# Kernel optimization log

Hardware: AMD Instinct MI355X
Metric: run time of the kernel (lower is better)

The kernel has to match this reference:

```python
import jax, jax.numpy as jnp
import numpy as np


def xenet_batch(x, a, e, sw, sb, aiw, aib, ajw, ajb, nw, nb, ew, eb):
    """Spektral XENetConvBatch: x (B,N,F), a (B,N,N), e (B,N,N,S)."""
    B, N, F = x.shape
    x_i = jnp.broadcast_to(x[:, :, None, :], (B, N, N, F))   # target node i per pair
    x_j = jnp.broadcast_to(x[:, None, :, :], (B, N, N, F))   # source node j per pair
    e_t = jnp.transpose(e, (0, 2, 1, 3))                      # reversed edge features
    stack = jnp.concatenate([x_i, x_j, e, e_t], axis=-1)      # (B,N,N,2F+2S)
    stack = jax.nn.relu(stack @ sw + sb)                      # stack MLP, (B,N,N,32)
    stack = stack * a[..., None]                              # mask/weight by adjacency
    att_i = jax.nn.sigmoid(stack @ aiw + aib)                 # incoming gate
    att_j = jax.nn.sigmoid(stack @ ajw + ajb)                 # outgoing gate
    agg_i = jnp.sum(att_i * stack, axis=2)                    # aggregate over sources j -> (B,N,32)
    agg_j = jnp.sum(att_j * stack, axis=1)                    # aggregate over targets i -> (B,N,32)
    x_out = jnp.concatenate([x, agg_i, agg_j], axis=-1) @ nw + nb  # node model (linear)
    e_out = stack @ ew + eb                                   # edge model (linear)
    return x_out, e_out


def setup_inputs() -> dict:
    key = jax.random.key(0)
    ks = jax.random.split(key, 16)
    B, N, F, S, C, L = 1, 400, 240, 1, 32, 1440
    SIN = 2 * F + 2 * S   # 482
    NIN = F + 2 * C       # 304
    s = 0.05
    inp = {
        "x": jax.random.normal(ks[0], (B, N, F), jnp.float32),
        "a": jax.random.uniform(ks[1], (B, N, N), jnp.float32),
        "e": jax.random.normal(ks[2], (B, N, N, S), jnp.float32),
        "c1_sw": jax.random.normal(ks[3], (SIN, C), jnp.float32) * s,
        "c1_sb": jnp.zeros((C,), jnp.float32),
        "c1_aiw": jax.random.normal(ks[4], (C, 1), jnp.float32) * s,
        "c1_aib": jnp.zeros((1,), jnp.float32),
        "c1_ajw": jax.random.normal(ks[5], (C, 1), jnp.float32) * s,
        "c1_ajb": jnp.zeros((1,), jnp.float32),
        "c1_nw": jax.random.normal(ks[6], (NIN, F), jnp.float32) * s,
        "c1_nb": jnp.zeros((F,), jnp.float32),
        "c1_ew": jax.random.normal(ks[7], (C, S), jnp.float32) * s,
        "c1_eb": jnp.zeros((S,), jnp.float32),
        "c2_sw": jax.random.normal(ks[8], (SIN, C), jnp.float32) * s,
        "c2_sb": jnp.zeros((C,), jnp.float32),
        "c2_aiw": jax.random.normal(ks[9], (C, 1), jnp.float32) * s,
        "c2_aib": jnp.zeros((1,), jnp.float32),
        "c2_ajw": jax.random.normal(ks[10], (C, 1), jnp.float32) * s,
        "c2_ajb": jnp.zeros((1,), jnp.float32),
        "c2_nw": jax.random.normal(ks[11], (NIN, F), jnp.float32) * s,
        "c2_nb": jnp.zeros((F,), jnp.float32),
        "c2_ew": jax.random.normal(ks[12], (C, S), jnp.float32) * s,
        "c2_eb": jnp.zeros((S,), jnp.float32),
        "dw": jax.random.normal(ks[13], (F, L), jnp.float32) * s,
        "db": jnp.zeros((L,), jnp.float32),
    }
    return inp


def reference(x, a, e,
              c1_sw, c1_sb, c1_aiw, c1_aib, c1_ajw, c1_ajb, c1_nw, c1_nb, c1_ew, c1_eb,
              c2_sw, c2_sb, c2_aiw, c2_aib, c2_ajw, c2_ajb, c2_nw, c2_nb, c2_ew, c2_eb,
              dw, db):
    x, e = xenet_batch(x, a, e, c1_sw, c1_sb, c1_aiw, c1_aib, c1_ajw, c1_ajb,
                       c1_nw, c1_nb, c1_ew, c1_eb)
    x, e = xenet_batch(x, a, e, c2_sw, c2_sb, c2_aiw, c2_aib, c2_ajw, c2_ajb,
                       c2_nw, c2_nb, c2_ew, c2_eb)
    return x @ dw + db  # (B, N, n_labels)
```

## Files before the change

### kernel.cpp

```cpp
#include <hip/hip_runtime.h>

#define NN 400
#define FF 240
#define CC 32
#define NIN 304
#define LL 1440

__global__ __launch_bounds__(256) void pq_kernel(
    const float* __restrict__ x, const float* __restrict__ sw,
    const float* __restrict__ sb, float* __restrict__ P, float* __restrict__ Q) {
    const int i   = blockIdx.x;
    const int t   = threadIdx.x;
    const int c   = t & 31;
    const int isQ = (t >> 5) & 1;
    const int g   = t >> 6;
    const float* wb = sw + (isQ ? FF * CC : 0) + c;
    float acc = (!isQ && g == 0) ? sb[c] : 0.0f;
    const float* xr = x + i * FF;
    const int f0 = g * 60;
    #pragma unroll 4
    for (int f = f0; f < f0 + 60; ++f) acc += xr[f] * wb[f * CC];
    __shared__ float red[4][64];
    red[g][t & 63] = acc;
    __syncthreads();
    if (t < 64) {
        const float s = red[0][t] + red[1][t] + red[2][t] + red[3][t];
        if (t >= 32) Q[i * CC + (t & 31)] = s;
        else         P[i * CC + t] = s;
    }
}

template<bool WRITE_E, bool DO_PQ>
__global__ __launch_bounds__(1024) void rcf_node(
    const float* __restrict__ P, const float* __restrict__ Q,
    const float* __restrict__ e, const float* __restrict__ a,
    const float* __restrict__ sw_tail,
    const float* __restrict__ aiw, const float* __restrict__ aib,
    const float* __restrict__ ajw, const float* __restrict__ ajb,
    const float* __restrict__ ew, const float* __restrict__ eb,
    float* __restrict__ e_out,
    const float* __restrict__ xin, const float* __restrict__ nw,
    const float* __restrict__ nb,
    const float* __restrict__ sw2, const float* __restrict__ sb2,
    float* __restrict__ xout, float* __restrict__ Pout, float* __restrict__ Qout) {
    const int bid = blockIdx.x;
    const int b   = (bid & 7) * 50 + (bid >> 3);
    const int t  = threadIdx.x;
    const int pg = t >> 3, l = t & 7, c0 = l * 4;

    __shared__ float smem[10272];
    float* red  = smem;
    float* v    = smem + 9216;
    float* xs   = smem + 9520;
    float* part = smem + 9760;
    float* redn = smem;
    float* red2 = smem;

    if (t < FF) v[t] = xin[b * FF + t];

    float e_f4[4], e_r4[4], a_bk4[4], a_kb4[4];
    int kk[4];
    #pragma unroll
    for (int it = 0; it < 4; ++it) {
        const int off = it * 128 + pg;
        kk[it] = (off < NN) ? off : 0;
        e_f4[it]  = e[b * NN + kk[it]];
        e_r4[it]  = e[kk[it] * NN + b];
        a_bk4[it] = a[b * NN + kk[it]];
        a_kb4[it] = a[kk[it] * NN + b];
    }

    float w1v[4], w2v[4], wiv[4], wjv[4], wev[4], Pb[4], Qb[4];
    *(float4*)w1v = *(const float4*)(sw_tail + c0);
    *(float4*)w2v = *(const float4*)(sw_tail + CC + c0);
    *(float4*)wiv = *(const float4*)(aiw + c0);
    *(float4*)wjv = *(const float4*)(ajw + c0);
    if (WRITE_E) *(float4*)wev = *(const float4*)(ew + c0);
    *(float4*)Pb = *(const float4*)(P + b * CC + c0);
    *(float4*)Qb = *(const float4*)(Q + b * CC + c0);
    const float bi = aib[0], bj = ajb[0];
    const float be = WRITE_E ? eb[0] : 0.0f;

    float acc_i[4] = {0, 0, 0, 0}, acc_j[4] = {0, 0, 0, 0};
    #pragma unroll
    for (int it = 0; it < 4; ++it) {
        const int off = it * 128 + pg;
        const bool valid = off < NN;
        const int k = kk[it];
        float Qk[4], Pk[4];
        *(float4*)Qk = *(const float4*)(Q + k * CC + c0);
        *(float4*)Pk = *(const float4*)(P + k * CC + c0);
        const float e_f = e_f4[it], e_r = e_r4[it];
        const float a_bk = a_bk4[it], a_kb = a_kb4[it];
        float sr[4], sc[4];
        #pragma unroll
        for (int q = 0; q < 4; ++q) {
            sr[q] = fmaxf(Pb[q] + Qk[q] + e_f * w1v[q] + e_r * w2v[q], 0.0f) * a_bk;
            sc[q] = fmaxf(Pk[q] + Qb[q] + e_r * w1v[q] + e_f * w2v[q], 0.0f) * a_kb;
        }
        float d_i = sr[0] * wiv[0] + sr[1] * wiv[1] + sr[2] * wiv[2] + sr[3] * wiv[3];
        float d_j = sc[0] * wjv[0] + sc[1] * wjv[1] + sc[2] * wjv[2] + sc[3] * wjv[3];
        float d_e = WRITE_E ? (sr[0] * wev[0] + sr[1] * wev[1] + sr[2] * wev[2] + sr[3] * wev[3]) : 0.0f;
        #pragma unroll
        for (int m = 1; m < 8; m <<= 1) {
            d_i += __shfl_xor(d_i, m);
            d_j += __shfl_xor(d_j, m);
            if (WRITE_E) d_e += __shfl_xor(d_e, m);
        }
        const float gi = valid ? __fdividef(1.0f, 1.0f + __expf(-(d_i + bi))) : 0.0f;
        const float gj = valid ? __fdividef(1.0f, 1.0f + __expf(-(d_j + bj))) : 0.0f;
        #pragma unroll
        for (int q = 0; q < 4; ++q) {
            acc_i[q] += gi * sr[q];
            acc_j[q] += gj * sc[q];
        }
        if (WRITE_E && l == 0 && valid) e_out[b * NN + k] = d_e + be;
    }
    #pragma unroll
    for (int q = 0; q < 4; ++q) {
        red[pg * 36 + c0 + q]          = acc_i[q];
        red[(128 + pg) * 36 + c0 + q]  = acc_j[q];
    }
    __syncthreads();
    if (t < 512) {
        const int c = t & 31, sg = (t >> 5) & 7, which = t >> 8;
        float s = 0.0f;
        #pragma unroll
        for (int g2 = sg * 16; g2 < sg * 16 + 16; ++g2)
            s += red[(which * 128 + g2) * 36 + c];
        part[t] = s;
    }
    __syncthreads();
    if (t < 64) {
        const int which = t >> 5, c = t & 31;
        float s = 0.0f;
        #pragma unroll
        for (int sg = 0; sg < 8; ++sg) s += part[which * 256 + sg * 32 + c];
        v[FF + t] = s;
    }
    __syncthreads();

    {
        const int fg = t % 60, h = t / 60;
        if (t < 960) {
            const int f0 = fg * 4;
            float4 acc = make_float4(0.f, 0.f, 0.f, 0.f);
            const int k0 = h * 19;
            #pragma unroll
            for (int k = k0; k < k0 + 19; ++k) {
                const float vk = v[k];
                const float4 w = *(const float4*)(nw + k * FF + f0);
                acc.x += vk * w.x; acc.y += vk * w.y;
                acc.z += vk * w.z; acc.w += vk * w.w;
            }
            *(float4*)(redn + h * 240 + f0) = acc;
        }
    }
    __syncthreads();
    if (t < FF) {
        float r = nb[t];
        #pragma unroll
        for (int h = 0; h < 16; ++h) r += redn[h * 240 + t];
        xout[b * FF + t] = r;
        xs[t] = r;
    }
    if (DO_PQ) {
        __syncthreads();
        const int c = t & 31, isQ = (t >> 5) & 1, g = t >> 6;
        const float* wb = sw2 + (isQ ? FF * CC : 0) + c;
        float acc = (!isQ && g == 0) ? sb2[c] : 0.0f;
        const int f0 = g * 15;
        #pragma unroll
        for (int f = f0; f < f0 + 15; ++f) acc += xs[f] * wb[f * CC];
        red2[g * 64 + (t & 63)] = acc;
        __syncthreads();
        if (t < 64) {
            float s = 0.0f;
            #pragma unroll
            for (int g2 = 0; g2 < 16; ++g2) s += red2[g2 * 64 + t];
            if (t >= 32) Qout[b * CC + (t & 31)] = s;
            else         Pout[b * CC + t] = s;
        }
    }
}

__global__ __launch_bounds__(256) void dense_kernel(
    const float* __restrict__ x, const float* __restrict__ dw,
    const float* __restrict__ db, float* __restrict__ out) {
    const int i0 = blockIdx.x * 8;
    const int l  = blockIdx.y * 256 + threadIdx.x;
    __shared__ float xs[8][FF];
    for (int idx = threadIdx.x; idx < 8 * FF; idx += 256) {
        const int r = idx / FF, f = idx - r * FF;
        xs[r][f] = x[(i0 + r) * FF + f];
    }
    __syncthreads();
    if (l < LL) {
        float a0 = db[l], a1 = a0, a2 = a0, a3 = a0;
        float a4 = a0, a5 = a0, a6 = a0, a7 = a0;
        #pragma unroll 4
        for (int f = 0; f < FF; ++f) {
            const float w = dw[f * LL + l];
            a0 += xs[0][f] * w;
            a1 += xs[1][f] * w;
            a2 += xs[2][f] * w;
            a3 += xs[3][f] * w;
            a4 += xs[4][f] * w;
            a5 += xs[5][f] * w;
            a6 += xs[6][f] * w;
            a7 += xs[7][f] * w;
        }
        out[(i0 + 0) * LL + l] = a0;
        out[(i0 + 1) * LL + l] = a1;
        out[(i0 + 2) * LL + l] = a2;
        out[(i0 + 3) * LL + l] = a3;
        out[(i0 + 4) * LL + l] = a4;
        out[(i0 + 5) * LL + l] = a5;
        out[(i0 + 6) * LL + l] = a6;
        out[(i0 + 7) * LL + l] = a7;
    }
}

extern "C" void kernel_launch(void* const* d_in, const int* in_sizes, int n_in,
                              void* d_out, int out_size, void* d_ws, size_t ws_size,
                              hipStream_t stream) {
    const float* x  = (const float*)d_in[0];
    const float* a  = (const float*)d_in[1];
    const float* e0 = (const float*)d_in[2];

    const float* c1_sw  = (const float*)d_in[3];
    const float* c1_sb  = (const float*)d_in[4];
    const float* c1_aiw = (const float*)d_in[5];
    const float* c1_aib = (const float*)d_in[6];
    const float* c1_ajw = (const float*)d_in[7];
    const float* c1_ajb = (const float*)d_in[8];
    const float* c1_nw  = (const float*)d_in[9];
    const float* c1_nb  = (const float*)d_in[10];
    const float* c1_ew  = (const float*)d_in[11];
    const float* c1_eb  = (const float*)d_in[12];

    const float* c2_sw  = (const float*)d_in[13];
    const float* c2_sb  = (const float*)d_in[14];
    const float* c2_aiw = (const float*)d_in[15];
    const float* c2_aib = (const float*)d_in[16];
    const float* c2_ajw = (const float*)d_in[17];
    const float* c2_ajb = (const float*)d_in[18];
    const float* c2_nw  = (const float*)d_in[19];
    const float* c2_nb  = (const float*)d_in[20];
    const float* dw = (const float*)d_in[23];
    const float* db = (const float*)d_in[24];

    float* ws = (float*)d_ws;
    float* P1 = ws;
    float* Q1 = ws + 12800;
    float* P2 = ws + 25600;
    float* Q2 = ws + 38400;
    float* x1 = ws + 51200;
    float* x2 = ws + 147200;
    float* e1 = ws + 243200;

    float* out = (float*)d_out;

    pq_kernel<<<NN, 256, 0, stream>>>(x, c1_sw, c1_sb, P1, Q1);

    rcf_node<true, true><<<NN, 1024, 0, stream>>>(
        P1, Q1, e0, a, c1_sw + 480 * CC,
        c1_aiw, c1_aib, c1_ajw, c1_ajb, c1_ew, c1_eb, e1,
        x, c1_nw, c1_nb, c2_sw, c2_sb, x1, P2, Q2);

    rcf_node<false, false><<<NN, 1024, 0, stream>>>(
        P2, Q2, e1, a, c2_sw + 480 * CC,
        c2_aiw, c2_aib, c2_ajw, c2_ajb, nullptr, nullptr, nullptr,
        x1, c2_nw, c2_nb, nullptr, nullptr, x2, nullptr, nullptr);

    dense_kernel<<<dim3(NN / 8, 6), 256, 0, stream>>>(x2, dw, db, out);
}
```

Measured before the change: 62.42 us.

## Process two nodes per block to share weight reads in node kernels

Each block of the PQ and fused edge/node kernels now handles two target nodes instead of one, halving grid size. The node-model and next-layer PQ weight loads are shared across both nodes, cutting global/L2 weight traffic per node. The edge aggregation phase runs sequentially for the two nodes with extra barriers, and fewer blocks may leave compute units idle.

```diff
diff --git a/kernel.cpp b/kernel.cpp
--- a/kernel.cpp
+++ b/kernel.cpp
@@ -9,24 +9,34 @@
 __global__ __launch_bounds__(256) void pq_kernel(
     const float* __restrict__ x, const float* __restrict__ sw,
     const float* __restrict__ sb, float* __restrict__ P, float* __restrict__ Q) {
-    const int i   = blockIdx.x;
+    const int i0  = blockIdx.x * 2;
     const int t   = threadIdx.x;
     const int c   = t & 31;
     const int isQ = (t >> 5) & 1;
     const int g   = t >> 6;
     const float* wb = sw + (isQ ? FF * CC : 0) + c;
-    float acc = (!isQ && g == 0) ? sb[c] : 0.0f;
-    const float* xr = x + i * FF;
+    const float bias = (!isQ && g == 0) ? sb[c] : 0.0f;
+    float accA = bias, accB = bias;
+    const float* xrA = x + i0 * FF;
+    const float* xrB = x + (i0 + 1) * FF;
     const int f0 = g * 60;
     #pragma unroll 4
-    for (int f = f0; f < f0 + 60; ++f) acc += xr[f] * wb[f * CC];
-    __shared__ float red[4][64];
-    red[g][t & 63] = acc;
+    for (int f = f0; f < f0 + 60; ++f) {
+        const float w = wb[f * CC];
+        accA += xrA[f] * w;
+        accB += xrB[f] * w;
+    }
+    __shared__ float red[4][128];
+    red[g][t & 63]        = accA;
+    red[g][64 + (t & 63)] = accB;
     __syncthreads();
-    if (t < 64) {
-        const float s = red[0][t] + red[1][t] + red[2][t] + red[3][t];
-        if (t >= 32) Q[i * CC + (t & 31)] = s;
-        else         P[i * CC + t] = s;
+    if (t < 128) {
+        const int row = t >> 6, slot = t & 63;
+        const float s = red[0][row * 64 + slot] + red[1][row * 64 + slot]
+                      + red[2][row * 64 + slot] + red[3][row * 64 + slot];
+        const int i = i0 + row;
+        if (slot >= 32) Q[i * CC + (slot & 31)] = s;
+        else            P[i * CC + slot] = s;
     }
 }
 
@@ -43,143 +53,170 @@
     const float* __restrict__ nb,
     const float* __restrict__ sw2, const float* __restrict__ sb2,
     float* __restrict__ xout, float* __restrict__ Pout, float* __restrict__ Qout) {
-    const int bid = blockIdx.x;
-    const int b   = (bid & 7) * 50 + (bid >> 3);
+    const int bid  = blockIdx.x;
+    const int base = (bid & 7) * 50 + (bid >> 3) * 2;
     const int t  = threadIdx.x;
     const int pg = t >> 3, l = t & 7, c0 = l * 4;
 
-    __shared__ float smem[10272];
+    __shared__ float smem[10816];
     float* red  = smem;
-    float* v    = smem + 9216;
-    float* xs   = smem + 9520;
-    float* part = smem + 9760;
+    float* vA   = smem + 9216;
+    float* vB   = smem + 9520;
+    float* xsA  = smem + 9824;
+    float* xsB  = smem + 10064;
+    float* part = smem + 10304;
     float* redn = smem;
     float* red2 = smem;
 
-    if (t < FF) v[t] = xin[b * FF + t];
-
-    float e_f4[4], e_r4[4], a_bk4[4], a_kb4[4];
-    int kk[4];
-    #pragma unroll
-    for (int it = 0; it < 4; ++it) {
-        const int off = it * 128 + pg;
-        kk[it] = (off < NN) ? off : 0;
-        e_f4[it]  = e[b * NN + kk[it]];
-        e_r4[it]  = e[kk[it] * NN + b];
-        a_bk4[it] = a[b * NN + kk[it]];
-        a_kb4[it] = a[kk[it] * NN + b];
-    }
-
-    float w1v[4], w2v[4], wiv[4], wjv[4], wev[4], Pb[4], Qb[4];
+    if (t < FF) {
+        vA[t] = xin[base * FF + t];
+        vB[t] = xin[(base + 1) * FF + t];
+    }
+
+    float w1v[4], w2v[4], wiv[4], wjv[4], wev[4];
     *(float4*)w1v = *(const float4*)(sw_tail + c0);
     *(float4*)w2v = *(const float4*)(sw_tail + CC + c0);
     *(float4*)wiv = *(const float4*)(aiw + c0);
     *(float4*)wjv = *(const float4*)(ajw + c0);
     if (WRITE_E) *(float4*)wev = *(const float4*)(ew + c0);
-    *(float4*)Pb = *(const float4*)(P + b * CC + c0);
-    *(float4*)Qb = *(const float4*)(Q + b * CC + c0);
     const float bi = aib[0], bj = ajb[0];
     const float be = WRITE_E ? eb[0] : 0.0f;
 
-    float acc_i[4] = {0, 0, 0, 0}, acc_j[4] = {0, 0, 0, 0};
-    #pragma unroll
-    for (int it = 0; it < 4; ++it) {
-        const int off = it * 128 + pg;
-        const bool valid = off < NN;
-        const int k = kk[it];
-        float Qk[4], Pk[4];
-        *(float4*)Qk = *(const float4*)(Q + k * CC + c0);
-        *(float4*)Pk = *(const float4*)(P + k * CC + c0);
-        const float e_f = e_f4[it], e_r = e_r4[it];
-        const float a_bk = a_bk4[it], a_kb = a_kb4[it];
-        float sr[4], sc[4];
+    for (int rp = 0; rp < 2; ++rp) {
+        const int b = base + rp;
+        float* vcur = rp ? vB : vA;
+
+        float e_f4[4], e_r4[4], a_bk4[4], a_kb4[4];
+        int kk[4];
+        #pragma unroll
+        for (int it = 0; it < 4; ++it) {
+            const int off = it * 128 + pg;
+            kk[it] = (off < NN) ? off : 0;
+            e_f4[it]  = e[b * NN + kk[it]];
+            e_r4[it]  = e[kk[it] * NN + b];
+            a_bk4[it] = a[b * NN + kk[it]];
+            a_kb4[it] = a[kk[it] * NN + b];
+        }
+
+        float Pb[4], Qb[4];
+        *(float4*)Pb = *(const float4*)(P + b * CC + c0);
+        *(float4*)Qb = *(const float4*)(Q + b * CC + c0);
+
+        float acc_i[4] = {0, 0, 0, 0}, acc_j[4] = {0, 0, 0, 0};
+        #pragma unroll
+        for (int it = 0; it < 4; ++it) {
+            const int off = it * 128 + pg;
+            const bool valid = off < NN;
+            const int k = kk[it];
+            float Qk[4], Pk[4];
+            *(float4*)Qk = *(const float4*)(Q + k * CC + c0);
+            *(float4*)Pk = *(const float4*)(P + k * CC + c0);
+            const float e_f = e_f4[it], e_r = e_r4[it];
+            const float a_bk = a_bk4[it], a_kb = a_kb4[it];
+            float sr[4], sc[4];
+            #pragma unroll
+            for (int q = 0; q < 4; ++q) {
+                sr[q] = fmaxf(Pb[q] + Qk[q] + e_f * w1v[q] + e_r * w2v[q], 0.0f) * a_bk;
+                sc[q] = fmaxf(Pk[q] + Qb[q] + e_r * w1v[q] + e_f * w2v[q], 0.0f) * a_kb;
+            }
+            float d_i = sr[0] * wiv[0] + sr[1] * wiv[1] + sr[2] * wiv[2] + sr[3] * wiv[3];
+            float d_j = sc[0] * wjv[0] + sc[1] * wjv[1] + sc[2] * wjv[2] + sc[3] * wjv[3];
+            float d_e = WRITE_E ? (sr[0] * wev[0] + sr[1] * wev[1] + sr[2] * wev[2] + sr[3] * wev[3]) : 0.0f;
+            #pragma unroll
+            for (int m = 1; m < 8; m <<= 1) {
+                d_i += __shfl_xor(d_i, m);
+                d_j += __shfl_xor(d_j, m);
+                if (WRITE_E) d_e += __shfl_xor(d_e, m);
+            }
+            const float gi = valid ? __fdividef(1.0f, 1.0f + __expf(-(d_i + bi))) : 0.0f;
+            const float gj = valid ? __fdividef(1.0f, 1.0f + __expf(-(d_j + bj))) : 0.0f;
+            #pragma unroll
+            for (int q = 0; q < 4; ++q) {
+                acc_i[q] += gi * sr[q];
+                acc_j[q] += gj * sc[q];
+            }
+            if (WRITE_E && l == 0 && valid) e_out[b * NN + k] = d_e + be;
+        }
         #pragma unroll
         for (int q = 0; q < 4; ++q) {
-            sr[q] = fmaxf(Pb[q] + Qk[q] + e_f * w1v[q] + e_r * w2v[q], 0.0f) * a_bk;
-            sc[q] = fmaxf(Pk[q] + Qb[q] + e_r * w1v[q] + e_f * w2v[q], 0.0f) * a_kb;
-        }
-        float d_i = sr[0] * wiv[0] + sr[1] * wiv[1] + sr[2] * wiv[2] + sr[3] * wiv[3];
-        float d_j = sc[0] * wjv[0] + sc[1] * wjv[1] + sc[2] * wjv[2] + sc[3] * wjv[3];
-        float d_e = WRITE_E ? (sr[0] * wev[0] + sr[1] * wev[1] + sr[2] * wev[2] + sr[3] * wev[3]) : 0.0f;
-        #pragma unroll
-        for (int m = 1; m < 8; m <<= 1) {
-            d_i += __shfl_xor(d_i, m);
-            d_j += __shfl_xor(d_j, m);
-            if (WRITE_E) d_e += __shfl_xor(d_e, m);
-        }
-        const float gi = valid ? __fdividef(1.0f, 1.0f + __expf(-(d_i + bi))) : 0.0f;
-        const float gj = valid ? __fdividef(1.0f, 1.0f + __expf(-(d_j + bj))) : 0.0f;
-        #pragma unroll
-        for (int q = 0; q < 4; ++q) {
-            acc_i[q] += gi * sr[q];
-            acc_j[q] += gj * sc[q];
-        }
-        if (WRITE_E && l == 0 && valid) e_out[b * NN + k] = d_e + be;
-    }
-    #pragma unroll
-    for (int q = 0; q < 4; ++q) {
-        red[pg * 36 + c0 + q]          = acc_i[q];
-        red[(128 + pg) * 36 + c0 + q]  = acc_j[q];
-    }
-    __syncthreads();
-    if (t < 512) {
-        const int c = t & 31, sg = (t >> 5) & 7, which = t >> 8;
-        float s = 0.0f;
-        #pragma unroll
-        for (int g2 = sg * 16; g2 < sg * 16 + 16; ++g2)
-            s += red[(which * 128 + g2) * 36 + c];
-        part[t] = s;
-    }
-    __syncthreads();
-    if (t < 64) {
-        const int which = t >> 5, c = t & 31;
-        float s = 0.0f;
-        #pragma unroll
-        for (int sg = 0; sg < 8; ++sg) s += part[which * 256 + sg * 32 + c];
-        v[FF + t] = s;
-    }
-    __syncthreads();
+            red[pg * 36 + c0 + q]          = acc_i[q];
+            red[(128 + pg) * 36 + c0 + q]  = acc_j[q];
+        }
+        __syncthreads();
+        if (t < 512) {
+            const int c = t & 31, sg = (t >> 5) & 7, which = t >> 8;
+            float s = 0.0f;
+            #pragma unroll
+            for (int g2 = sg * 16; g2 < sg * 16 + 16; ++g2)
+                s += red[(which * 128 + g2) * 36 + c];
+            part[t] = s;
+        }
+        __syncthreads();
+        if (t < 64) {
+            const int which = t >> 5, c = t & 31;
+            float s = 0.0f;
+            #pragma unroll
+            for (int sg = 0; sg < 8; ++sg) s += part[which * 256 + sg * 32 + c];
+            vcur[FF + t] = s;
+        }
+        __syncthreads();
+    }
 
     {
         const int fg = t % 60, h = t / 60;
         if (t < 960) {
             const int f0 = fg * 4;
-            float4 acc = make_float4(0.f, 0.f, 0.f, 0.f);
+            float4 aA = make_float4(0.f, 0.f, 0.f, 0.f);
+            float4 aB = make_float4(0.f, 0.f, 0.f, 0.f);
             const int k0 = h * 19;
             #pragma unroll
             for (int k = k0; k < k0 + 19; ++k) {
-                const float vk = v[k];
                 const float4 w = *(const float4*)(nw + k * FF + f0);
-                acc.x += vk * w.x; acc.y += vk * w.y;
-                acc.z += vk * w.z; acc.w += vk * w.w;
+                const float va = vA[k], vb = vB[k];
+                aA.x += va * w.x; aA.y += va * w.y; aA.z += va * w.z; aA.w += va * w.w;
+                aB.x += vb * w.x; aB.y += vb * w.y; aB.z += vb * w.z; aB.w += vb * w.w;
             }
-            *(float4*)(redn + h * 240 + f0) = acc;
+            *(float4*)(redn + h * 240 + f0)        = aA;
+            *(float4*)(redn + 3840 + h * 240 + f0) = aB;
         }
     }
     __syncthreads();
     if (t < FF) {
-        float r = nb[t];
-        #pragma unroll
-        for (int h = 0; h < 16; ++h) r += redn[h * 240 + t];
-        xout[b * FF + t] = r;
-        xs[t] = r;
+        float rA = nb[t], rB = nb[t];
+        #pragma unroll
+        for (int h = 0; h < 16; ++h) {
+            rA += redn[h * 240 + t];
+            rB += redn[3840 + h * 240 + t];
+        }
+        xout[base * FF + t]       = rA;
+        xout[(base + 1) * FF + t] = rB;
+        xsA[t] = rA;
+        xsB[t] = rB;
     }
     if (DO_PQ) {
         __syncthreads();
         const int c = t & 31, isQ = (t >> 5) & 1, g = t >> 6;
         const float* wb = sw2 + (isQ ? FF * CC : 0) + c;
-        float acc = (!isQ && g == 0) ? sb2[c] : 0.0f;
+        const float bias = (!isQ && g == 0) ? sb2[c] : 0.0f;
+        float accA = bias, accB = bias;
         const int f0 = g * 15;
         #pragma unroll
-        for (int f = f0; f < f0 + 15; ++f) acc += xs[f] * wb[f * CC];
-        red2[g * 64 + (t & 63)] = acc;
-        __syncthreads();
-        if (t < 64) {
+        for (int f = f0; f < f0 + 15; ++f) {
+            const float w = wb[f * CC];
+            accA += xsA[f] * w;
+            accB += xsB[f] * w;
+        }
+        red2[g * 64 + (t & 63)]        = accA;
+        red2[1024 + g * 64 + (t & 63)] = accB;
+        __syncthreads();
+        if (t < 128) {
+            const int row = t >> 6, slot = t & 63;
             float s = 0.0f;
             #pragma unroll
-            for (int g2 = 0; g2 < 16; ++g2) s += red2[g2 * 64 + t];
-            if (t >= 32) Qout[b * CC + (t & 31)] = s;
-            else         Pout[b * CC + t] = s;
+            for (int g2 = 0; g2 < 16; ++g2) s += red2[row * 1024 + g2 * 64 + slot];
+            const int bb = base + row;
+            if (slot >= 32) Qout[bb * CC + (slot & 31)] = s;
+            else            Pout[bb * CC + slot] = s;
         }
     }
 }
@@ -261,14 +298,14 @@
 
     float* out = (float*)d_out;
 
-    pq_kernel<<<NN, 256, 0, stream>>>(x, c1_sw, c1_sb, P1, Q1);
-
-    rcf_node<true, true><<<NN, 1024, 0, stream>>>(
+    pq_kernel<<<NN / 2, 256, 0, stream>>>(x, c1_sw, c1_sb, P1, Q1);
+
+    rcf_node<true, true><<<NN / 2, 1024, 0, stream>>>(
         P1, Q1, e0, a, c1_sw + 480 * CC,
         c1_aiw, c1_aib, c1_ajw, c1_ajb, c1_ew, c1_eb, e1,
         x, c1_nw, c1_nb, c2_sw, c2_sb, x1, P2, Q2);
 
-    rcf_node<false, false><<<NN, 1024, 0, stream>>>(
+    rcf_node<false, false><<<NN / 2, 1024, 0, stream>>>(
         P2, Q2, e1, a, c2_sw + 480 * CC,
         c2_aiw, c2_aib, c2_ajw, c2_ajb, nullptr, nullptr, nullptr,
         x1, c2_nw, c2_nb, nullptr, nullptr, x2, nullptr, nullptr);
```

Measured after the change: 63.82 us. +2.2%, slower.
